# Performance work log

Hardware: AMD Instinct MI355X
Metric: run time of the kernel (lower is better)

Reference implementation:

```python
import jax, jax.numpy as jnp
import numpy as np

D = 256; NH = 8; NL = 4; NP = 4; DFF = 1024
SHAPES = [(100, 100), (50, 50), (25, 25), (13, 13)]
B = 4


def layer_norm(x, g, b, eps=1e-5):
    m = x.mean(-1, keepdims=True)
    v = ((x - m) ** 2).mean(-1, keepdims=True)
    return (x - m) * jax.lax.rsqrt(v + eps) * g + b


def setup_inputs() -> dict:
    key = jax.random.key(0)
    ks = jax.random.split(key, 12)
    Lin = sum(h * w for h, w in SHAPES)  # 13294
    w = lambda k, s: jax.random.normal(k, s, jnp.float32) * 0.02
    return dict(
        src=jax.random.normal(ks[0], (B, Lin, D), jnp.float32),
        pos=0.1 * jax.random.normal(ks[1], (B, Lin, D), jnp.float32),
        reference_points=jax.random.uniform(ks[2], (B, Lin, NL, 2), dtype=jnp.float32),
        spatial_shapes=jnp.array(SHAPES, jnp.int32),
        level_start_index=jnp.array(np.cumsum([0] + [h * w for h, w in SHAPES])[:-1], jnp.int32),
        value_w=w(ks[3], (D, D)), value_b=jnp.zeros((D,), jnp.float32),
        offs_w=w(ks[4], (D, NH * NL * NP * 2)),
        offs_b=0.5 * jax.random.normal(ks[5], (NH * NL * NP * 2,), jnp.float32),
        attn_w=w(ks[6], (D, NH * NL * NP)), attn_b=jnp.zeros((NH * NL * NP,), jnp.float32),
        out_w=w(ks[7], (D, D)), out_b=jnp.zeros((D,), jnp.float32),
        ln1_g=jnp.ones((D,), jnp.float32), ln1_b=jnp.zeros((D,), jnp.float32),
        ff1_w=w(ks[8], (D, DFF)), ff1_b=jnp.zeros((DFF,), jnp.float32),
        ff2_w=w(ks[9], (DFF, D)), ff2_b=jnp.zeros((D,), jnp.float32),
        ln2_g=jnp.ones((D,), jnp.float32), ln2_b=jnp.zeros((D,), jnp.float32),
    )


def msda(query, value_in, ref, shapes, starts, value_w, value_b, offs_w, offs_b,
         attn_w, attn_b, out_w, out_b):
    Bq, Lq, Dm = query.shape
    dh = Dm // NH
    shapes_np = np.asarray(shapes); starts_np = np.asarray(starts)
    value = (value_in @ value_w + value_b).reshape(Bq, -1, NH, dh)
    offs = (query @ offs_w + offs_b).reshape(Bq, Lq, NH, NL, NP, 2)
    aw = jax.nn.softmax((query @ attn_w + attn_b).reshape(Bq, Lq, NH, NL * NP), axis=-1)
    aw = aw.reshape(Bq, Lq, NH, NL, NP)
    # offset normalizer is (W, H) per level
    normalizer = jnp.stack([shapes[:, 1], shapes[:, 0]], -1).astype(jnp.float32)
    loc = ref[:, :, None, :, None, :] + offs / normalizer[None, None, None, :, None, :]
    out = jnp.zeros((Bq, NH, Lq, dh), jnp.float32)
    for l in range(NL):
        Hl, Wl = int(shapes_np[l, 0]), int(shapes_np[l, 1])
        s = int(starts_np[l])
        v = value[:, s:s + Hl * Wl].transpose(0, 2, 1, 3)  # [B,h,HW,dh]
        x = loc[:, :, :, l, :, 0] * Wl - 0.5  # [B,Lq,h,P], align_corners=False
        y = loc[:, :, :, l, :, 1] * Hl - 0.5
        x0 = jnp.floor(x); y0 = jnp.floor(y)
        dx = x - x0; dy = y - y0
        x0i = x0.astype(jnp.int32); y0i = y0.astype(jnp.int32)
        def gather(ix, iy):
            valid = (ix >= 0) & (ix < Wl) & (iy >= 0) & (iy < Hl)  # zero padding
            idx = jnp.clip(iy, 0, Hl - 1) * Wl + jnp.clip(ix, 0, Wl - 1)
            idx = idx.transpose(0, 2, 1, 3).reshape(Bq, NH, Lq * NP)
            g = jnp.take_along_axis(v, idx[..., None], axis=2).reshape(Bq, NH, Lq, NP, dh)
            return g * valid.transpose(0, 2, 1, 3)[..., None]
        dxh = dx.transpose(0, 2, 1, 3)[..., None]
        dyh = dy.transpose(0, 2, 1, 3)[..., None]
        sampled = (gather(x0i, y0i) * (1 - dxh) * (1 - dyh)
                   + gather(x0i + 1, y0i) * dxh * (1 - dyh)
                   + gather(x0i, y0i + 1) * (1 - dxh) * dyh
                   + gather(x0i + 1, y0i + 1) * dxh * dyh)  # [B,h,Lq,P,dh]
        awl = aw[:, :, :, l].transpose(0, 2, 1, 3)[..., None]  # [B,h,Lq,P,1]
        out = out + (sampled * awl).sum(3)
    out = out.transpose(0, 2, 1, 3).reshape(Bq, Lq, Dm)
    return out @ out_w + out_b


def reference(src, pos, reference_points, spatial_shapes, level_start_index,
              value_w, value_b, offs_w, offs_b, attn_w, attn_b, out_w, out_b,
              ln1_g, ln1_b, ff1_w, ff1_b, ff2_w, ff2_b, ln2_g, ln2_b):
    # src = with_pos_embed(src, pos): NOTE this module uses (src + pos) as BOTH query and value
    q = src + pos
    src2 = msda(q, q, reference_points, spatial_shapes, level_start_index,
                value_w, value_b, offs_w, offs_b, attn_w, attn_b, out_w, out_b)
    x = layer_norm(q + src2, ln1_g, ln1_b)  # dropout is identity at eval
    ff = jnp.maximum(x @ ff1_w + ff1_b, 0.0) @ ff2_w + ff2_b
    return layer_norm(x + ff, ln2_g, ln2_b)
```

## Files before the change

### kernel.cpp

```cpp
#include <hip/hip_runtime.h>
#include <hip/hip_bf16.h>

#define B_    4
#define LIN   13294
#define M_    (B_*LIN)
#define D_    256
#define NH_   8
#define NL_   4
#define NP_   4
#define DFF_  1024

typedef __bf16 bf16;
typedef unsigned int uint;
typedef __attribute__((ext_vector_type(8))) __bf16 bfrag8;
typedef __attribute__((ext_vector_type(4))) __bf16 bf16x4;
typedef __attribute__((ext_vector_type(4))) float facc4;
typedef __attribute__((ext_vector_type(2))) float f32x2;

__global__ __launch_bounds__(256) void make_q(const float* __restrict__ src,
                                              const float* __restrict__ pos,
                                              float* __restrict__ q,
                                              bf16* __restrict__ qb, int n4) {
  int i = blockIdx.x * 256 + threadIdx.x;
  if (i >= n4) return;
  float4 s = ((const float4*)src)[i];
  float4 p = ((const float4*)pos)[i];
  float4 v = {s.x + p.x, s.y + p.y, s.z + p.z, s.w + p.w};
  ((float4*)q)[i] = v;
  bf16 t4[4] = {(bf16)v.x, (bf16)v.y, (bf16)v.z, (bf16)v.w};
  ((uint2*)qb)[i] = *(uint2*)t4;
}

__global__ __launch_bounds__(256) void prep_weights(
    const float* __restrict__ vw, const float* __restrict__ ow,
    const float* __restrict__ aw, const float* __restrict__ outw,
    const float* __restrict__ f1w, const float* __restrict__ f2w,
    const float* __restrict__ vb, const float* __restrict__ ob,
    const float* __restrict__ ab,
    bf16* __restrict__ vowt, bf16* __restrict__ outwt,
    bf16* __restrict__ f1wt, bf16* __restrict__ f2wt, float* __restrict__ vobias) {
  int seg = blockIdx.y;
  int idx = blockIdx.x * 256 + threadIdx.x;
  if (seg == 6) {
    if (idx < 256) vobias[idx] = vb[idx];
    else if (idx < 512) vobias[idx] = ob[idx - 256];
    else if (idx < 640) vobias[idx] = ab[idx - 512];
    return;
  }
  const float* W; bf16* Wt; int K, N;
  switch (seg) {
    case 0: W = vw;   Wt = vowt;              K = 256;  N = 256;  break;
    case 1: W = ow;   Wt = vowt + 256 * 256;  K = 256;  N = 256;  break;
    case 2: W = aw;   Wt = vowt + 512 * 256;  K = 256;  N = 128;  break;
    case 3: W = outw; Wt = outwt;             K = 256;  N = 256;  break;
    case 4: W = f1w;  Wt = f1wt;              K = 256;  N = 1024; break;
    default: W = f2w; Wt = f2wt;              K = 1024; N = 256;  break;
  }
  if (idx < K * N) {
    int n = idx / K, k = idx - n * K;
    Wt[idx] = (bf16)W[k * N + n];
  }
}

__device__ __forceinline__ void gload16(const bf16* g, bf16* l) {
  __builtin_amdgcn_global_load_lds(
      (const __attribute__((address_space(1))) uint*)g,
      (__attribute__((address_space(3))) uint*)l, 16, 0, 0);
}

template<int K, bool RELU>
__global__ __launch_bounds__(256) void gemm128(
    const bf16* __restrict__ A, const bf16* __restrict__ Bt,
    const float* __restrict__ bias, bf16* __restrict__ C,
    int Mdim, int N) {
  __shared__ __align__(16) bf16 As[128 * 64];
  __shared__ __align__(16) bf16 Bs[128 * 64];
  const int t = threadIdx.x, wave = t >> 6, lane = t & 63;
  const int m0 = blockIdx.x * 128, n0 = blockIdx.y * 128;
  const int wr = wave >> 1, wc = wave & 1;
  const int ln = lane & 15, quad = lane >> 4;
  const int sr = lane >> 3, cc = lane & 7;
  const int gcol = (cc ^ sr) * 8;

  const bf16* ap[4]; const bf16* bp[4];
  bf16* la[4]; bf16* lb[4];
  #pragma unroll
  for (int ii = 0; ii < 4; ii++) {
    int i = wave * 4 + ii;
    int arow = min(m0 + i * 8 + sr, Mdim - 1);
    ap[ii] = A + (size_t)arow * K + gcol;
    bp[ii] = Bt + (size_t)(n0 + i * 8 + sr) * K + gcol;
    la[ii] = As + i * 512;
    lb[ii] = Bs + i * 512;
  }
  int a_off[4], b_off[4];
  #pragma unroll
  for (int i = 0; i < 4; i++) {
    int ra = wr * 64 + i * 16 + ln;
    int rb = wc * 64 + i * 16 + ln;
    a_off[i] = ra * 128 + ((quad ^ (ra & 7)) * 16);
    b_off[i] = rb * 128 + ((quad ^ (rb & 7)) * 16);
  }

  facc4 acc[4][4];
  #pragma unroll
  for (int mt = 0; mt < 4; mt++)
    #pragma unroll
    for (int nt = 0; nt < 4; nt++) acc[mt][nt] = (facc4){0.f, 0.f, 0.f, 0.f};

  #pragma unroll 1
  for (int k0 = 0; k0 < K; k0 += 64) {
    __syncthreads();
    gload16(ap[0] + k0, la[0]); gload16(ap[1] + k0, la[1]);
    gload16(ap[2] + k0, la[2]); gload16(ap[3] + k0, la[3]);
    gload16(bp[0] + k0, lb[0]); gload16(bp[1] + k0, lb[1]);
    gload16(bp[2] + k0, lb[2]); gload16(bp[3] + k0, lb[3]);
    __syncthreads();
    #pragma unroll
    for (int ks = 0; ks < 2; ks++) {
      bfrag8 wfr[4], xfr[4];
      #pragma unroll
      for (int nt = 0; nt < 4; nt++)
        wfr[nt] = *(const bfrag8*)((const char*)Bs + (b_off[nt] ^ (ks * 64)));
      #pragma unroll
      for (int mt = 0; mt < 4; mt++)
        xfr[mt] = *(const bfrag8*)((const char*)As + (a_off[mt] ^ (ks * 64)));
      #pragma unroll
      for (int mt = 0; mt < 4; mt++)
        #pragma unroll
        for (int nt = 0; nt < 4; nt++)
          acc[mt][nt] = __builtin_amdgcn_mfma_f32_16x16x32_bf16(wfr[nt], xfr[mt], acc[mt][nt], 0, 0, 0);
    }
  }

  #pragma unroll
  for (int nt = 0; nt < 4; nt++) {
    int ncol = n0 + wc * 64 + nt * 16 + quad * 4;
    float4 bv = *(const float4*)&bias[ncol];
    #pragma unroll
    for (int mt = 0; mt < 4; mt++) {
      int row = m0 + wr * 64 + mt * 16 + ln;
      if (row < Mdim) {
        float v0 = acc[mt][nt][0] + bv.x, v1 = acc[mt][nt][1] + bv.y;
        float v2 = acc[mt][nt][2] + bv.z, v3 = acc[mt][nt][3] + bv.w;
        if (RELU) {
          v0 = fmaxf(v0, 0.f); v1 = fmaxf(v1, 0.f);
          v2 = fmaxf(v2, 0.f); v3 = fmaxf(v3, 0.f);
        }
        bf16 o[4] = {(bf16)v0, (bf16)v1, (bf16)v2, (bf16)v3};
        *(uint2*)&C[(size_t)row * N + ncol] = *(uint2*)o;
      }
    }
  }
}

__global__ __launch_bounds__(256) void msda_sample(
    const bf16* __restrict__ VOA,
    const float* __restrict__ ref,
    bf16* __restrict__ sampled) {
  int gw = (blockIdx.x * 256 + threadIdx.x) >> 6;
  int lane = threadIdx.x & 63;
  int m = gw >> 3, h = gw & 7;
  if (m >= M_) return;
  int b = m / LIN;
  int p = lane >> 2, cg = lane & 3;
  int l = p >> 2, pt = p & 3;
  int Wl = (l == 0) ? 100 : (l == 1) ? 50 : (l == 2) ? 25 : 13;
  int Hl = Wl;
  int st = (l == 0) ? 0 : (l == 1) ? 10000 : (l == 2) ? 12500 : 13125;

  const bf16* row = VOA + (size_t)m * 640;
  float e = __expf((float)row[512 + h * 16 + p]);
  float se = e;
  #pragma unroll
  for (int msk = 4; msk < 64; msk <<= 1) se += __shfl_xor(se, msk);
  float w = e / se;

  float rx = ref[((size_t)m * 4 + l) * 2 + 0];
  float ry = ref[((size_t)m * 4 + l) * 2 + 1];
  uint oxy = *(const uint*)&row[256 + ((h * 4 + l) * 4 + pt) * 2];
  float ox = __uint_as_float(oxy << 16);
  float oy = __uint_as_float(oxy & 0xffff0000u);
  float x = rx * (float)Wl + ox - 0.5f;
  float y = ry * (float)Hl + oy - 0.5f;
  float x0f = floorf(x), y0f = floorf(y);
  float dx = x - x0f, dy = y - y0f;
  int x0 = (int)x0f, y0 = (int)y0f;
  float wx1 = 1.f - dx, wy1 = 1.f - dy;

  f32x2 acc2[4];
  #pragma unroll
  for (int i = 0; i < 4; i++) acc2[i] = (f32x2){0.f, 0.f};

  size_t vbase = ((size_t)(b * LIN + st)) * 640 + h * 32 + cg * 8;
  #pragma unroll
  for (int c = 0; c < 4; c++) {
    int cx = c & 1, cy = c >> 1;
    int xi = x0 + cx, yi = y0 + cy;
    bool valid = (xi >= 0) & (xi < Wl) & (yi >= 0) & (yi < Hl);
    int xc = min(max(xi, 0), Wl - 1);
    int yc = min(max(yi, 0), Hl - 1);
    float cw = (cx ? dx : wx1) * (cy ? dy : wy1) * w;
    cw = valid ? cw : 0.f;
    uint off = (uint)(yc * Wl + xc) * 640u;
    const uint4 vv = *(const uint4*)(VOA + vbase + off);
    f32x2 cw2 = {cw, cw};
    f32x2 v0 = {__uint_as_float(vv.x << 16), __uint_as_float(vv.x & 0xffff0000u)};
    f32x2 v1 = {__uint_as_float(vv.y << 16), __uint_as_float(vv.y & 0xffff0000u)};
    f32x2 v2 = {__uint_as_float(vv.z << 16), __uint_as_float(vv.z & 0xffff0000u)};
    f32x2 v3 = {__uint_as_float(vv.w << 16), __uint_as_float(vv.w & 0xffff0000u)};
    acc2[0] = cw2 * v0 + acc2[0];
    acc2[1] = cw2 * v1 + acc2[1];
    acc2[2] = cw2 * v2 + acc2[2];
    acc2[3] = cw2 * v3 + acc2[3];
  }

  int sel = (lane >> 2) & 1;
  f32x2 sA0 = sel ? acc2[0] : acc2[2];
  f32x2 sA1 = sel ? acc2[1] : acc2[3];
  f32x2 kA0 = sel ? acc2[2] : acc2[0];
  f32x2 kA1 = sel ? acc2[3] : acc2[1];
  f32x2 rA0, rA1;
  rA0.x = __shfl_xor(sA0.x, 4); rA0.y = __shfl_xor(sA0.y, 4);
  rA1.x = __shfl_xor(sA1.x, 4); rA1.y = __shfl_xor(sA1.y, 4);
  kA0 += rA0; kA1 += rA1;

  int sel2 = (lane >> 3) & 1;
  f32x2 sB = sel2 ? kA0 : kA1;
  f32x2 kB = sel2 ? kA1 : kA0;
  f32x2 rB;
  rB.x = __shfl_xor(sB.x, 8); rB.y = __shfl_xor(sB.y, 8);
  kB += rB;

  int sel3 = (lane >> 4) & 1;
  float sC = sel3 ? kB.x : kB.y;
  float kC = sel3 ? kB.y : kB.x;
  kC += __shfl_xor(sC, 16);

  float v = kC + __shfl_xor(kC, 32);

  if (lane < 32) {
    int c = cg * 8 + ((lane >> 2) & 1) * 4 + ((lane >> 3) & 1) * 2 + ((lane >> 4) & 1);
    sampled[(size_t)m * 256 + h * 32 + c] = (bf16)v;
  }
}

__device__ inline float4 load4f(const float* p) { return *(const float4*)p; }
__device__ inline float4 load4f(const bf16* p) {
  bf16x4 v = *(const bf16x4*)p;
  float4 r = {(float)v[0], (float)v[1], (float)v[2], (float)v[3]};
  return r;
}
template<typename RT>
__global__ __launch_bounds__(256) void ln_kernel(
    const bf16* __restrict__ a, const RT* __restrict__ res,
    const float* __restrict__ g, const float* __restrict__ beta,
    float* __restrict__ out_f, bf16* __restrict__ out_b, int Mdim) {
  int wave = threadIdx.x >> 6, lane = threadIdx.x & 63;
  int row = blockIdx.x * 4 + wave;
  if (row >= Mdim) return;
  size_t base = (size_t)row * 256 + lane * 4;
  float4 av = load4f(a + base);
  float4 rv = load4f(res + base);
  float4 v = {av.x + rv.x, av.y + rv.y, av.z + rv.z, av.w + rv.w};
  float s = v.x + v.y + v.z + v.w;
  #pragma unroll
  for (int msk = 1; msk < 64; msk <<= 1) s += __shfl_xor(s, msk);
  float mean = s * (1.f / 256.f);
  float4 d = {v.x - mean, v.y - mean, v.z - mean, v.w - mean};
  float sq = d.x * d.x + d.y * d.y + d.z * d.z + d.w * d.w;
  #pragma unroll
  for (int msk = 1; msk < 64; msk <<= 1) sq += __shfl_xor(sq, msk);
  float inv = rsqrtf(sq * (1.f / 256.f) + 1e-5f);
  float4 gv = *(const float4*)(g + lane * 4);
  float4 bv = *(const float4*)(beta + lane * 4);
  float4 y = {d.x * inv * gv.x + bv.x, d.y * inv * gv.y + bv.y,
              d.z * inv * gv.z + bv.z, d.w * inv * gv.w + bv.w};
  if (out_f) *(float4*)(out_f + base) = y;
  if (out_b) {
    bf16 t4[4] = {(bf16)y.x, (bf16)y.y, (bf16)y.z, (bf16)y.w};
    *(uint2*)(out_b + base) = *(uint2*)t4;
  }
}

extern "C" void kernel_launch(void* const* d_in, const int* in_sizes, int n_in,
                              void* d_out, int out_size, void* d_ws, size_t ws_size,
                              hipStream_t stream) {
  const float* src     = (const float*)d_in[0];
  const float* pos     = (const float*)d_in[1];
  const float* refpts  = (const float*)d_in[2];
  const float* value_w = (const float*)d_in[5];
  const float* value_b = (const float*)d_in[6];
  const float* offs_w  = (const float*)d_in[7];
  const float* offs_b  = (const float*)d_in[8];
  const float* attn_w  = (const float*)d_in[9];
  const float* attn_b  = (const float*)d_in[10];
  const float* out_w   = (const float*)d_in[11];
  const float* out_b   = (const float*)d_in[12];
  const float* ln1_g   = (const float*)d_in[13];
  const float* ln1_b   = (const float*)d_in[14];
  const float* ff1_w   = (const float*)d_in[15];
  const float* ff1_b   = (const float*)d_in[16];
  const float* ff2_w   = (const float*)d_in[17];
  const float* ff2_b   = (const float*)d_in[18];
  const float* ln2_g   = (const float*)d_in[19];
  const float* ln2_b   = (const float*)d_in[20];

  char* ws = (char*)d_ws;
  size_t off = 0;
  auto take = [&](size_t bytes) -> char* {
    char* pp = ws + off;
    off += (bytes + 255) & ~(size_t)255;
    return pp;
  };
  float* q      = (float*)take((size_t)M_ * 256 * 4);
  size_t szQB   = (size_t)M_ * 256 * 2;
  size_t szVOA  = (size_t)M_ * 640 * 2;
  char* R       = take(szQB + szVOA + szQB);
  bf16* qb      = (bf16*)R;
  bf16* VOA     = (bf16*)(R + szQB);
  bf16* sampled = (bf16*)(R + szQB + szVOA);
  bf16* hb      = (bf16*)R;
  bf16* tmp     = (bf16*)take(szQB);
  bf16* x       = (bf16*)take(szQB);
  bf16* vowt    = (bf16*)take(640 * 256 * 2);
  bf16* outwt   = (bf16*)take(65536 * 2);
  bf16* f1wt    = (bf16*)take(262144 * 2);
  bf16* f2wt    = (bf16*)take(262144 * 2);
  float* vobias = (float*)take(640 * 4);
  (void)ws_size; (void)in_sizes; (void)n_in; (void)out_size;

  int n4 = M_ * 256 / 4;
  make_q<<<dim3((n4 + 255) / 256), dim3(256), 0, stream>>>(src, pos, q, qb, n4);
  prep_weights<<<dim3(1024, 7), dim3(256), 0, stream>>>(
      value_w, offs_w, attn_w, out_w, ff1_w, ff2_w, value_b, offs_b, attn_b,
      vowt, outwt, f1wt, f2wt, vobias);

  dim3 blk(256);
  int mt = (M_ + 127) / 128;
  gemm128<256, false><<<dim3(mt, 5), blk, 0, stream>>>(qb, vowt, vobias, VOA, M_, 640);
  msda_sample<<<dim3(M_ * 2), blk, 0, stream>>>(VOA, refpts, sampled);
  gemm128<256, false><<<dim3(mt, 2), blk, 0, stream>>>(sampled, outwt, out_b, tmp, M_, 256);
  ln_kernel<float><<<dim3((M_ + 3) / 4), blk, 0, stream>>>(tmp, q, ln1_g, ln1_b, nullptr, x, M_);
  gemm128<256, true><<<dim3(mt, 8), blk, 0, stream>>>(x, f1wt, ff1_b, hb, M_, 1024);
  gemm128<1024, false><<<dim3(mt, 2), blk, 0, stream>>>(hb, f2wt, ff2_b, tmp, M_, 256);
  ln_kernel<bf16><<<dim3((M_ + 3) / 4), blk, 0, stream>>>(tmp, x, ln2_g, ln2_b, (float*)d_out, nullptr, M_);
}
```

Measured before the change: 590.0 us.

## Fuse FFN up and down projections into one kernel keeping hidden in LDS

Replaces the two FFN GEMM launches with a single kernel. For each 64-row tile it computes 64-column chunks of relu(x·W1+b1), stages each chunk in swizzled, double-buffered shared memory, and accumulates it straight into the W2 output. This removes the round trip of the 53k×1024 bf16 hidden tensor through global memory. In exchange, weights are read directly from global/L2 without LDS tiling, and occupancy is one block per CU with a barrier on every chunk, so compute efficiency could drop.

```diff
diff --git a/kernel.cpp b/kernel.cpp
--- a/kernel.cpp
+++ b/kernel.cpp
@@ -149,6 +149,106 @@
         }
         bf16 o[4] = {(bf16)v0, (bf16)v1, (bf16)v2, (bf16)v3};
         *(uint2*)&C[(size_t)row * N + ncol] = *(uint2*)o;
+      }
+    }
+  }
+}
+
+__global__ __launch_bounds__(256, 1) void ffn_fused(
+    const bf16* __restrict__ X,
+    const bf16* __restrict__ W1t,
+    const bf16* __restrict__ W2t,
+    const float* __restrict__ b1,
+    const float* __restrict__ b2,
+    bf16* __restrict__ Y, int Mdim) {
+  __shared__ __align__(16) bf16 hb[2][64 * 64];
+  const int wave = threadIdx.x >> 6, lane = threadIdx.x & 63;
+  const int ln = lane & 15, quad = lane >> 4;
+  const int m0 = blockIdx.x * 64;
+
+  const bf16* xp = X + (size_t)min(m0 + wave * 16 + ln, Mdim - 1) * 256 + quad * 8;
+  bfrag8 xf[8];
+  #pragma unroll
+  for (int ks = 0; ks < 8; ks++) xf[ks] = *(const bfrag8*)(xp + ks * 32);
+
+  facc4 yacc[4][4];
+  #pragma unroll
+  for (int mt = 0; mt < 4; mt++)
+    #pragma unroll
+    for (int nt = 0; nt < 4; nt++) yacc[mt][nt] = (facc4){0.f, 0.f, 0.f, 0.f};
+
+  const bf16* w1p = W1t + (size_t)ln * 256 + quad * 8;
+  const bf16* w2p = W2t + (size_t)(wave * 64 + ln) * 1024 + quad * 8;
+
+  const int hrow = wave * 16 + ln;
+  int woff[4];
+  #pragma unroll
+  for (int nt = 0; nt < 4; nt++)
+    woff[nt] = hrow * 128 + (((nt * 2 + (quad >> 1)) ^ (hrow & 7)) * 16) + (quad & 1) * 8;
+
+  #pragma unroll 1
+  for (int c = 0; c < 16; c++) {
+    facc4 hacc[4];
+    #pragma unroll
+    for (int nt = 0; nt < 4; nt++) hacc[nt] = (facc4){0.f, 0.f, 0.f, 0.f};
+    #pragma unroll
+    for (int ks = 0; ks < 8; ks++) {
+      #pragma unroll
+      for (int nt = 0; nt < 4; nt++) {
+        bfrag8 w1f = *(const bfrag8*)(w1p + (size_t)(c * 64 + nt * 16) * 256 + ks * 32);
+        hacc[nt] = __builtin_amdgcn_mfma_f32_16x16x32_bf16(w1f, xf[ks], hacc[nt], 0, 0, 0);
+      }
+    }
+    char* hbuf = (char*)&hb[c & 1][0];
+    #pragma unroll
+    for (int nt = 0; nt < 4; nt++) {
+      float4 bv = *(const float4*)&b1[c * 64 + nt * 16 + quad * 4];
+      float v0 = fmaxf(hacc[nt][0] + bv.x, 0.f);
+      float v1 = fmaxf(hacc[nt][1] + bv.y, 0.f);
+      float v2 = fmaxf(hacc[nt][2] + bv.z, 0.f);
+      float v3 = fmaxf(hacc[nt][3] + bv.w, 0.f);
+      bf16 o[4] = {(bf16)v0, (bf16)v1, (bf16)v2, (bf16)v3};
+      *(uint2*)(hbuf + woff[nt]) = *(uint2*)o;
+    }
+    asm volatile("s_waitcnt lgkmcnt(0)" ::: "memory");
+    __builtin_amdgcn_s_barrier();
+    asm volatile("" ::: "memory");
+
+    bfrag8 w2f[2][4], hf[2][4];
+    #pragma unroll
+    for (int ks = 0; ks < 2; ks++)
+      #pragma unroll
+      for (int nt = 0; nt < 4; nt++)
+        w2f[ks][nt] = *(const bfrag8*)(w2p + (size_t)nt * 16 * 1024 + c * 64 + ks * 32);
+    #pragma unroll
+    for (int ks = 0; ks < 2; ks++)
+      #pragma unroll
+      for (int mt = 0; mt < 4; mt++) {
+        int r = mt * 16 + ln;
+        hf[ks][mt] = *(const bfrag8*)(hbuf + r * 128 + (((ks * 4 + quad) ^ (r & 7)) * 16));
+      }
+    #pragma unroll
+    for (int ks = 0; ks < 2; ks++)
+      #pragma unroll
+      for (int mt = 0; mt < 4; mt++)
+        #pragma unroll
+        for (int nt = 0; nt < 4; nt++)
+          yacc[mt][nt] = __builtin_amdgcn_mfma_f32_16x16x32_bf16(w2f[ks][nt], hf[ks][mt], yacc[mt][nt], 0, 0, 0);
+    asm volatile("" ::: "memory");
+  }
+
+  #pragma unroll
+  for (int nt = 0; nt < 4; nt++) {
+    int ncol = wave * 64 + nt * 16 + quad * 4;
+    float4 bv = *(const float4*)&b2[ncol];
+    #pragma unroll
+    for (int mt = 0; mt < 4; mt++) {
+      int row = m0 + mt * 16 + ln;
+      if (row < Mdim) {
+        float v0 = yacc[mt][nt][0] + bv.x, v1 = yacc[mt][nt][1] + bv.y;
+        float v2 = yacc[mt][nt][2] + bv.z, v3 = yacc[mt][nt][3] + bv.w;
+        bf16 o[4] = {(bf16)v0, (bf16)v1, (bf16)v2, (bf16)v3};
+        *(uint2*)&Y[(size_t)row * 256 + ncol] = *(uint2*)o;
       }
     }
   }
@@ -320,7 +420,6 @@
   bf16* qb      = (bf16*)R;
   bf16* VOA     = (bf16*)(R + szQB);
   bf16* sampled = (bf16*)(R + szQB + szVOA);
-  bf16* hb      = (bf16*)R;
   bf16* tmp     = (bf16*)take(szQB);
   bf16* x       = (bf16*)take(szQB);
   bf16* vowt    = (bf16*)take(640 * 256 * 2);
@@ -342,7 +441,7 @@
   msda_sample<<<dim3(M_ * 2), blk, 0, stream>>>(VOA, refpts, sampled);
   gemm128<256, false><<<dim3(mt, 2), blk, 0, stream>>>(sampled, outwt, out_b, tmp, M_, 256);
   ln_kernel<float><<<dim3((M_ + 3) / 4), blk, 0, stream>>>(tmp, q, ln1_g, ln1_b, nullptr, x, M_);
-  gemm128<256, true><<<dim3(mt, 8), blk, 0, stream>>>(x, f1wt, ff1_b, hb, M_, 1024);
-  gemm128<1024, false><<<dim3(mt, 2), blk, 0, stream>>>(hb, f2wt, ff2_b, tmp, M_, 256);
+  int fb = (M_ + 63) / 64;
+  ffn_fused<<<dim3(fb), blk, 0, stream>>>(x, f1wt, f2wt, ff1_b, ff2_b, tmp, M_);
   ln_kernel<bf16><<<dim3((M_ + 3) / 4), blk, 0, stream>>>(tmp, x, ln2_g, ln2_b, (float*)d_out, nullptr, M_);
 }
```

New measurement: 756.6 us. 1.28x slower.
